# Kernel tuning notes

Hardware: AMD Instinct MI355X
Metric: run time of the kernel (lower is better)

Reference implementation:

```python
import jax, jax.numpy as jnp
import numpy as np

N_NODES = 100000
N_EDGES = 1600000
IN_CH = 128
OUT_CH = 64
H1 = 4 * OUT_CH  # 256
H2 = 2 * OUT_CH  # 128


def setup_inputs() -> dict:
    key = jax.random.key(0)
    ks = jax.random.split(key, 6)
    x = jax.random.normal(ks[0], (N_NODES, IN_CH), dtype=jnp.float32)
    edge_index = jax.random.randint(ks[1], (2, N_EDGES), 0, N_NODES, dtype=jnp.int64)
    # Glorot-style init for the three GCNConv weight matrices
    W1 = jax.random.normal(ks[2], (IN_CH, H1), dtype=jnp.float32) / np.sqrt(IN_CH)
    W2 = jax.random.normal(ks[3], (H1, H2), dtype=jnp.float32) / np.sqrt(H1)
    W3 = jax.random.normal(ks[4], (H2, OUT_CH), dtype=jnp.float32) / np.sqrt(H2)
    b1 = jnp.zeros((H1,), jnp.float32)
    b2 = jnp.zeros((H2,), jnp.float32)
    b3 = jnp.zeros((OUT_CH,), jnp.float32)
    return {"x": x, "edge_index": edge_index, "W1": W1, "b1": b1,
            "W2": W2, "b2": b2, "W3": W3, "b3": b3}


def reference(x, edge_index, W1, b1, W2, b2, W3, b3):
    N = x.shape[0]
    # GCNConv semantics (PyG defaults): add self-loops, symmetric D^-1/2 A D^-1/2 norm.
    loops = jnp.arange(N, dtype=edge_index.dtype)
    src = jnp.concatenate([edge_index[0], loops])  # message sources
    dst = jnp.concatenate([edge_index[1], loops])  # aggregation targets
    deg = jax.ops.segment_sum(jnp.ones_like(dst, x.dtype), dst, num_segments=N)
    dinv = jax.lax.rsqrt(jnp.maximum(deg, 1.0))  # deg >= 1 due to self-loops
    norm = dinv[src] * dinv[dst]  # [E+N] per-edge normalization

    def gcn(h, W, b):
        h = h @ W                                   # dense transform first
        msg = h[src] * norm[:, None]                # gather + normalize
        return jax.ops.segment_sum(msg, dst, num_segments=N) + b

    h = gcn(x, W1, b1)
    h = jax.nn.relu(gcn(h, W2, b2))
    return gcn(h, W3, b3)
```

## Files before the change

### kernel.cpp

```cpp
#include <hip/hip_runtime.h>
#include <cstddef>
#include <cstdint>

#define NND 100000
#define NED 1600000
#define NEP (NED + NND)
#define NPB 256
#define NBK ((NND + NPB - 1) / NPB)
#define ECH 2048

typedef short v8s __attribute__((ext_vector_type(8)));
typedef float v4f __attribute__((ext_vector_type(4)));

__device__ __forceinline__ uint32_t f32_to_bf16_rne(float x) {
    uint32_t u = __builtin_bit_cast(uint32_t, x);
    return (u + 0x7fffu + ((u >> 16) & 1u)) >> 16;
}
__device__ __forceinline__ float bf16bits_to_f32(uint32_t b) {
    return __builtin_bit_cast(float, b << 16);
}

__global__ void k_detect(const long long* __restrict__ ei, int* __restrict__ flag) {
    __shared__ int ok;
    if (threadIdx.x == 0) ok = 1;
    __syncthreads();
    for (int i = threadIdx.x; i < 2048; i += blockDim.x) {
        long long v = ei[i];
        if (v < 0 || v >= NND) ok = 0;
    }
    __syncthreads();
    if (threadIdx.x == 0) *flag = ok;
}

__device__ __forceinline__ void load_edge(const void* ei, int is64, int e, int& src, int& dst) {
    if (e >= NED) { src = dst = e - NED; return; }
    if (is64) {
        const long long* p = (const long long*)ei;
        src = (int)p[e];
        dst = (int)p[NED + e];
    } else {
        const int* p = (const int*)ei;
        src = p[e];
        dst = p[NED + e];
    }
}

__global__ __launch_bounds__(256) void k_bcount(const void* __restrict__ ei,
                                                const int* __restrict__ flag,
                                                int* __restrict__ bcnt) {
    __shared__ int cnt[NBK];
    const int t = threadIdx.x;
    for (int j = t; j < NBK; j += 256) cnt[j] = 0;
    __syncthreads();
    const int is64 = *flag;
    const int e0 = blockIdx.x * ECH;
#pragma unroll
    for (int i = 0; i < 8; ++i) {
        int e = e0 + t + i * 256;
        if (e < NEP) {
            int s, d;
            load_edge(ei, is64, e, s, d);
            atomicAdd(&cnt[d >> 8], 1);
        }
    }
    __syncthreads();
    for (int j = t; j < NBK; j += 256)
        if (cnt[j]) atomicAdd(&bcnt[j], cnt[j]);
}

__global__ __launch_bounds__(512) void k_bscan(const int* __restrict__ bcnt,
                                               int* __restrict__ boff,
                                               int* __restrict__ bcur) {
    __shared__ int sh[512];
    const int t = threadIdx.x;
    int v = (t < NBK) ? bcnt[t] : 0;
    sh[t] = v;
    __syncthreads();
    for (int off = 1; off < 512; off <<= 1) {
        int u = 0;
        if (t >= off) u = sh[t - off];
        __syncthreads();
        sh[t] += u;
        __syncthreads();
    }
    if (t < NBK) {
        int e = sh[t] - v;
        boff[t] = e;
        bcur[t] = e;
    }
    if (t == NBK) boff[NBK] = NEP;
}

__global__ __launch_bounds__(256) void k_bscatter(const void* __restrict__ ei,
                                                  const int* __restrict__ flag,
                                                  int* __restrict__ bcur,
                                                  uint2* __restrict__ pairs) {
    __shared__ int cnt[NBK];
    __shared__ int res[NBK];
    const int t = threadIdx.x;
    for (int j = t; j < NBK; j += 256) cnt[j] = 0;
    __syncthreads();
    const int is64 = *flag;
    const int e0 = blockIdx.x * ECH;
    int se[8], de[8], rk[8];
#pragma unroll
    for (int i = 0; i < 8; ++i) {
        int e = e0 + t + i * 256;
        if (e < NEP) {
            load_edge(ei, is64, e, se[i], de[i]);
            rk[i] = atomicAdd(&cnt[de[i] >> 8], 1);
        } else {
            de[i] = -1;
        }
    }
    __syncthreads();
    for (int j = t; j < NBK; j += 256) {
        int c = cnt[j];
        if (c) res[j] = atomicAdd(&bcur[j], c);
    }
    __syncthreads();
#pragma unroll
    for (int i = 0; i < 8; ++i) {
        if (de[i] >= 0) {
            int pos = res[de[i] >> 8] + rk[i];
            pairs[pos] = make_uint2((unsigned)se[i], (unsigned)de[i]);
        }
    }
}

__global__ __launch_bounds__(256) void k_bcsr(const uint2* __restrict__ pairs,
                                              const int* __restrict__ boff,
                                              int* __restrict__ row_off,
                                              float* __restrict__ dinv,
                                              int* __restrict__ col) {
    __shared__ int deg[NPB];
    __shared__ int off[NPB];
    __shared__ int cur[NPB];
    const int b = blockIdx.x;
    const int t = threadIdx.x;
    const int node0 = b * NPB;
    const int es = boff[b], ee = boff[b + 1];

    deg[t] = 0;
    __syncthreads();
    for (int e = es + t; e < ee; e += 256) {
        uint2 p = pairs[e];
        atomicAdd(&deg[p.y - node0], 1);
    }
    __syncthreads();
    int v = deg[t];
    off[t] = v;
    __syncthreads();
    for (int o = 1; o < 256; o <<= 1) {
        int u = 0;
        if (t >= o) u = off[t - o];
        __syncthreads();
        off[t] += u;
        __syncthreads();
    }
    const int excl = off[t] - v;
    const int node = node0 + t;
    if (node <= NND) row_off[node] = es + excl;
    if (node < NND) {
        int dd = v < 1 ? 1 : v;
        dinv[node] = 1.0f / sqrtf((float)dd);
    }
    cur[t] = es + excl;
    __syncthreads();
    for (int e = es + t; e < ee; e += 256) {
        uint2 p = pairs[e];
        int pos = atomicAdd(&cur[p.y - node0], 1);
        col[pos] = (int)p.x;
    }
}

__global__ void k_wcombsplit(const float* __restrict__ W1, const float* __restrict__ W2,
                             const float* __restrict__ b1, unsigned short* __restrict__ wtCh,
                             unsigned short* __restrict__ wtCl, float* __restrict__ bc) {
    const int j = threadIdx.x;
    const int i = blockIdx.x;
    const float* rowv = (i < 128) ? (W1 + (size_t)i * 256) : b1;
    float acc = 0.f;
    for (int k = 0; k < 256; ++k) acc = fmaf(rowv[k], W2[(size_t)k * 128 + j], acc);
    if (i < 128) {
        uint32_t hi = f32_to_bf16_rne(acc);
        float resid = acc - bf16bits_to_f32(hi);
        uint32_t lo = f32_to_bf16_rne(resid);
        wtCh[(size_t)j * 128 + i] = (unsigned short)hi;
        wtCl[(size_t)j * 128 + i] = (unsigned short)lo;
    } else {
        bc[j] = acc;
    }
}

__global__ void k_wprep(const float* __restrict__ W, unsigned short* __restrict__ wth,
                        unsigned short* __restrict__ wtl, int K, int N) {
    int i = blockIdx.x * 256 + threadIdx.x;
    if (i >= K * N) return;
    int k = i / N, n = i % N;
    float x = W[i];
    uint32_t hi = f32_to_bf16_rne(x);
    float resid = x - bf16bits_to_f32(hi);
    uint32_t lo = f32_to_bf16_rne(resid);
    wth[(size_t)n * K + k] = (unsigned short)hi;
    wtl[(size_t)n * K + k] = (unsigned short)lo;
}

template <int C, bool BIAS, bool RELU, bool OUT_SPLIT>
__global__ __launch_bounds__(C) void k_agg(const float* __restrict__ in, float* __restrict__ out,
                      const int* __restrict__ row_off, const int* __restrict__ col,
                      const float* __restrict__ dinv, const float* __restrict__ bias,
                      unsigned short* __restrict__ outh, unsigned short* __restrict__ outl) {
    constexpr int LPG = C / 4;
    constexpr int NG = 4;
    constexpr int MAXE = 256;
    __shared__ int sidx[MAXE];
    __shared__ float snrm[MAXE];
    __shared__ float4 red[NG][LPG];

    const int n = blockIdx.x;
    const int t = threadIdx.x;
    const int g = t / LPG;
    const int l = t % LPG;
    const int s = row_off[n], e = row_off[n + 1];
    const float4* __restrict__ in4 = (const float4*)in;

    float4 a0 = make_float4(0.f, 0.f, 0.f, 0.f);
    float4 a1 = make_float4(0.f, 0.f, 0.f, 0.f);
    float4 a2 = make_float4(0.f, 0.f, 0.f, 0.f);
    float4 a3 = make_float4(0.f, 0.f, 0.f, 0.f);

    for (int base = s; base < e; base += MAXE) {
        const int cnt = min(e - base, MAXE);
        for (int i = t; i < cnt; i += C) {
            int c = col[base + i];
            sidx[i] = c;
            snrm[i] = dinv[c];
        }
        __syncthreads();

        int k = g;
        for (; k + 3 * NG < cnt; k += 4 * NG) {
            int s0 = sidx[k];
            int s1 = sidx[k + NG];
            int s2 = sidx[k + 2 * NG];
            int s3 = sidx[k + 3 * NG];
            float d0 = snrm[k];
            float d1 = snrm[k + NG];
            float d2 = snrm[k + 2 * NG];
            float d3 = snrm[k + 3 * NG];
            float4 v0 = in4[(size_t)s0 * LPG + l];
            float4 v1 = in4[(size_t)s1 * LPG + l];
            float4 v2 = in4[(size_t)s2 * LPG + l];
            float4 v3 = in4[(size_t)s3 * LPG + l];
            a0.x = fmaf(d0, v0.x, a0.x); a0.y = fmaf(d0, v0.y, a0.y);
            a0.z = fmaf(d0, v0.z, a0.z); a0.w = fmaf(d0, v0.w, a0.w);
            a1.x = fmaf(d1, v1.x, a1.x); a1.y = fmaf(d1, v1.y, a1.y);
            a1.z = fmaf(d1, v1.z, a1.z); a1.w = fmaf(d1, v1.w, a1.w);
            a2.x = fmaf(d2, v2.x, a2.x); a2.y = fmaf(d2, v2.y, a2.y);
            a2.z = fmaf(d2, v2.z, a2.z); a2.w = fmaf(d2, v2.w, a2.w);
            a3.x = fmaf(d3, v3.x, a3.x); a3.y = fmaf(d3, v3.y, a3.y);
            a3.z = fmaf(d3, v3.z, a3.z); a3.w = fmaf(d3, v3.w, a3.w);
        }
        for (; k < cnt; k += NG) {
            int s0 = sidx[k];
            float d0 = snrm[k];
            float4 v0 = in4[(size_t)s0 * LPG + l];
            a0.x = fmaf(d0, v0.x, a0.x); a0.y = fmaf(d0, v0.y, a0.y);
            a0.z = fmaf(d0, v0.z, a0.z); a0.w = fmaf(d0, v0.w, a0.w);
        }
        __syncthreads();
    }

    a0.x += a1.x + a2.x + a3.x;
    a0.y += a1.y + a2.y + a3.y;
    a0.z += a1.z + a2.z + a3.z;
    a0.w += a1.w + a2.w + a3.w;
    red[g][l] = a0;
    __syncthreads();
    if (g == 0) {
        float4 r = red[0][l];
        float4 r1 = red[1][l];
        float4 r2 = red[2][l];
        float4 r3 = red[3][l];
        r.x += r1.x + r2.x + r3.x;
        r.y += r1.y + r2.y + r3.y;
        r.z += r1.z + r2.z + r3.z;
        r.w += r1.w + r2.w + r3.w;
        float dn = dinv[n];
        r.x *= dn; r.y *= dn; r.z *= dn; r.w *= dn;
        if constexpr (BIAS) {
            float4 bv = ((const float4*)bias)[l];
            r.x += bv.x; r.y += bv.y; r.z += bv.z; r.w += bv.w;
        }
        if constexpr (RELU) {
            r.x = fmaxf(r.x, 0.f); r.y = fmaxf(r.y, 0.f);
            r.z = fmaxf(r.z, 0.f); r.w = fmaxf(r.w, 0.f);
        }
        if constexpr (OUT_SPLIT) {
            uint32_t h0 = f32_to_bf16_rne(r.x), h1 = f32_to_bf16_rne(r.y);
            uint32_t h2 = f32_to_bf16_rne(r.z), h3 = f32_to_bf16_rne(r.w);
            uint32_t l0 = f32_to_bf16_rne(r.x - bf16bits_to_f32(h0));
            uint32_t l1 = f32_to_bf16_rne(r.y - bf16bits_to_f32(h1));
            uint32_t l2 = f32_to_bf16_rne(r.z - bf16bits_to_f32(h2));
            uint32_t l3 = f32_to_bf16_rne(r.w - bf16bits_to_f32(h3));
            uint2 oh = make_uint2(h0 | (h1 << 16), h2 | (h3 << 16));
            uint2 ol = make_uint2(l0 | (l1 << 16), l2 | (l3 << 16));
            *(uint2*)(outh + (size_t)n * C + l * 4) = oh;
            *(uint2*)(outl + (size_t)n * C + l * 4) = ol;
        } else {
            ((float4*)out)[(size_t)n * LPG + l] = r;
        }
    }
}

template <int K, int N, int WN, int WM, bool BIAS, bool OUT_SPLIT>
__global__ __launch_bounds__(WN * WM * 64, 3) void k_mgemm(
    const unsigned short* __restrict__ acth, const unsigned short* __restrict__ actl,
    const unsigned short* __restrict__ wth, const unsigned short* __restrict__ wtl,
    const float* __restrict__ bias, float* __restrict__ outf,
    unsigned short* __restrict__ outh, unsigned short* __restrict__ outl, int nrows)
{
    constexpr int BM = 64;
    constexpr int BK = 128;
    constexpr int NCH = K / BK;
    constexpr int KC = BK / 32;
    constexpr int KP = BK + 8;
    constexpr int NTW = N / (WN * 16);
    constexpr int RT = 4 / WM;
    constexpr int NTHR = WN * WM * 64;
    constexpr int CHUNKS = BM * BK / 8;

    __shared__ unsigned short sh[2][BM][KP];

    const int tid = threadIdx.x;
    const int lane = tid & 63;
    const int wave = tid >> 6;
    const int wn = wave % WN;
    const int wm = wave / WN;
    const int l15 = lane & 15;
    const int lq = lane >> 4;
    const int r0 = blockIdx.x * BM;
    const int ncol0 = wn * NTW * 16;

    v8s wh[NTW][K / 32], wl[NTW][K / 32];
#pragma unroll
    for (int nt = 0; nt < NTW; ++nt) {
        const size_t nrow = (size_t)(ncol0 + nt * 16 + l15) * K;
#pragma unroll
        for (int kk = 0; kk < K / 32; ++kk) {
            wh[nt][kk] = *(const v8s*)(wth + nrow + kk * 32 + lq * 8);
            wl[nt][kk] = *(const v8s*)(wtl + nrow + kk * 32 + lq * 8);
        }
    }

    v4f acc[RT][NTW];
#pragma unroll
    for (int rt = 0; rt < RT; ++rt)
#pragma unroll
        for (int nt = 0; nt < NTW; ++nt) acc[rt][nt] = (v4f){0.f, 0.f, 0.f, 0.f};

#pragma unroll
    for (int ch = 0; ch < NCH; ++ch) {
        if (ch) __syncthreads();
        for (int i = tid; i < 2 * CHUNKS; i += NTHR) {
            const int plane = i >= CHUNKS;
            const int j = plane ? i - CHUNKS : i;
            const int r = j / (BK / 8);
            const int c = (j % (BK / 8)) * 8;
            int gr = r0 + r;
            if (gr >= nrows) gr = nrows - 1;
            const unsigned short* src = (plane ? actl : acth) + (size_t)gr * K + ch * BK + c;
            *(v8s*)(&sh[plane][r][c]) = *(const v8s*)src;
        }
        __syncthreads();

#pragma unroll
        for (int kc = 0; kc < KC; ++kc) {
#pragma unroll
            for (int rt = 0; rt < RT; ++rt) {
                const int row = (wm * RT + rt) * 16 + l15;
                const v8s ah = *(const v8s*)(&sh[0][row][kc * 32 + lq * 8]);
                const v8s al = *(const v8s*)(&sh[1][row][kc * 32 + lq * 8]);
                const int kk = ch * KC + kc;
#pragma unroll
                for (int nt = 0; nt < NTW; ++nt) {
                    acc[rt][nt] = __builtin_amdgcn_mfma_f32_16x16x32_bf16(wh[nt][kk], ah, acc[rt][nt], 0, 0, 0);
                    acc[rt][nt] = __builtin_amdgcn_mfma_f32_16x16x32_bf16(wh[nt][kk], al, acc[rt][nt], 0, 0, 0);
                    acc[rt][nt] = __builtin_amdgcn_mfma_f32_16x16x32_bf16(wl[nt][kk], ah, acc[rt][nt], 0, 0, 0);
                }
            }
        }
    }

#pragma unroll
    for (int rt = 0; rt < RT; ++rt) {
        const int m = r0 + (wm * RT + rt) * 16 + l15;
        if (m >= nrows) continue;
#pragma unroll
        for (int nt = 0; nt < NTW; ++nt) {
            const int nc = ncol0 + nt * 16 + lq * 4;
            v4f v = acc[rt][nt];
            if constexpr (BIAS) {
                float4 bv = *(const float4*)(bias + nc);
                v[0] += bv.x; v[1] += bv.y; v[2] += bv.z; v[3] += bv.w;
            }
            if constexpr (OUT_SPLIT) {
                uint32_t h0 = f32_to_bf16_rne(v[0]), h1 = f32_to_bf16_rne(v[1]);
                uint32_t h2 = f32_to_bf16_rne(v[2]), h3 = f32_to_bf16_rne(v[3]);
                uint32_t l0 = f32_to_bf16_rne(v[0] - bf16bits_to_f32(h0));
                uint32_t l1 = f32_to_bf16_rne(v[1] - bf16bits_to_f32(h1));
                uint32_t l2 = f32_to_bf16_rne(v[2] - bf16bits_to_f32(h2));
                uint32_t l3 = f32_to_bf16_rne(v[3] - bf16bits_to_f32(h3));
                *(uint2*)(outh + (size_t)m * N + nc) = make_uint2(h0 | (h1 << 16), h2 | (h3 << 16));
                *(uint2*)(outl + (size_t)m * N + nc) = make_uint2(l0 | (l1 << 16), l2 | (l3 << 16));
            } else {
                *(float4*)(outf + (size_t)m * N + nc) = make_float4(v[0], v[1], v[2], v[3]);
            }
        }
    }
}

extern "C" void kernel_launch(void* const* d_in, const int* in_sizes, int n_in,
                              void* d_out, int out_size, void* d_ws, size_t ws_size,
                              hipStream_t stream) {
    const float* x = (const float*)d_in[0];
    const void* ei = d_in[1];
    const float* W1 = (const float*)d_in[2];
    const float* b1 = (const float*)d_in[3];
    const float* W2 = (const float*)d_in[4];
    const float* b2 = (const float*)d_in[5];
    const float* W3 = (const float*)d_in[6];
    const float* b3 = (const float*)d_in[7];
    float* out = (float*)d_out;

    char* ws = (char*)d_ws;
    size_t off = 0;
    auto alloc = [&](size_t bytes) -> void* {
        void* p = ws + off;
        off = (off + bytes + 255) & ~(size_t)255;
        return p;
    };

    int* flag = (int*)alloc(sizeof(int));
    int* bcnt = (int*)alloc((size_t)NBK * 4);
    int* boff = (int*)alloc((size_t)(NBK + 1) * 4);
    int* bcur = (int*)alloc((size_t)NBK * 4);
    int* row_off = (int*)alloc((size_t)(NND + 1) * 4);
    float* dinv = (float*)alloc((size_t)NND * 4);
    int* col = (int*)alloc((size_t)NEP * 4);
    uint2* pairs = (uint2*)alloc((size_t)NEP * 8);
    float* bc = (float*)alloc((size_t)128 * 4);
    unsigned short* wtCh = (unsigned short*)alloc((size_t)128 * 128 * 2);
    unsigned short* wtCl = (unsigned short*)alloc((size_t)128 * 128 * 2);
    unsigned short* wt3h = (unsigned short*)alloc((size_t)128 * 64 * 2);
    unsigned short* wt3l = (unsigned short*)alloc((size_t)128 * 64 * 2);
    unsigned short* AXh = (unsigned short*)alloc((size_t)NND * 128 * 2 * 2);
    unsigned short* AXl = AXh + (size_t)NND * 128;
    float* H2 = (float*)alloc((size_t)NND * 128 * 4);
    unsigned short* A2h = AXh;
    unsigned short* A2l = AXl;
    float* H3 = H2;

    hipMemsetAsync(bcnt, 0, (size_t)NBK * 4, stream);

    k_detect<<<1, 256, 0, stream>>>((const long long*)ei, flag);

    const int gB = (NEP + ECH - 1) / ECH;
    k_bcount<<<gB, 256, 0, stream>>>(ei, flag, bcnt);
    k_bscan<<<1, 512, 0, stream>>>(bcnt, boff, bcur);
    k_bscatter<<<gB, 256, 0, stream>>>(ei, flag, bcur, pairs);
    k_bcsr<<<NBK, 256, 0, stream>>>(pairs, boff, row_off, dinv, col);

    k_wcombsplit<<<129, 128, 0, stream>>>(W1, W2, b1, wtCh, wtCl, bc);
    k_wprep<<<(128 * 64 + 255) / 256, 256, 0, stream>>>(W3, wt3h, wt3l, 128, 64);

    const int gT = (NND + 63) / 64;

    k_agg<128, false, false, true><<<NND, 128, 0, stream>>>(x, nullptr, row_off, col, dinv, nullptr, AXh, AXl);
    k_mgemm<128, 128, 8, 1, true, false><<<gT, 512, 0, stream>>>(AXh, AXl, wtCh, wtCl, bc, H2, nullptr, nullptr, NND);

    k_agg<128, true, true, true><<<NND, 128, 0, stream>>>(H2, nullptr, row_off, col, dinv, b2, A2h, A2l);

    k_mgemm<128, 64, 4, 2, false, false><<<gT, 512, 0, stream>>>(A2h, A2l, wt3h, wt3l, nullptr, H3, nullptr, nullptr, NND);
    k_agg<64, true, false, false><<<NND, 64, 0, stream>>>(H3, out, row_off, col, dinv, b3, nullptr, nullptr);
}
```

Baseline: 444.0 us.

## Widen final aggregation blocks, cache bucket pairs in LDS, double edge chunk size

```diff
diff --git a/kernel.cpp b/kernel.cpp
--- a/kernel.cpp
+++ b/kernel.cpp
@@ -7,7 +7,8 @@
 #define NEP (NED + NND)
 #define NPB 256
 #define NBK ((NND + NPB - 1) / NPB)
-#define ECH 2048
+#define ECH 4096
+#define MAXB 5120
 
 typedef short v8s __attribute__((ext_vector_type(8)));
 typedef float v4f __attribute__((ext_vector_type(4)));
@@ -55,7 +56,7 @@
     const int is64 = *flag;
     const int e0 = blockIdx.x * ECH;
 #pragma unroll
-    for (int i = 0; i < 8; ++i) {
+    for (int i = 0; i < ECH / 256; ++i) {
         int e = e0 + t + i * 256;
         if (e < NEP) {
             int s, d;
@@ -97,14 +98,15 @@
                                                   uint2* __restrict__ pairs) {
     __shared__ int cnt[NBK];
     __shared__ int res[NBK];
+    constexpr int EPT = ECH / 256;
     const int t = threadIdx.x;
     for (int j = t; j < NBK; j += 256) cnt[j] = 0;
     __syncthreads();
     const int is64 = *flag;
     const int e0 = blockIdx.x * ECH;
-    int se[8], de[8], rk[8];
-#pragma unroll
-    for (int i = 0; i < 8; ++i) {
+    int se[EPT], de[EPT], rk[EPT];
+#pragma unroll
+    for (int i = 0; i < EPT; ++i) {
         int e = e0 + t + i * 256;
         if (e < NEP) {
             load_edge(ei, is64, e, se[i], de[i]);
@@ -120,7 +122,7 @@
     }
     __syncthreads();
 #pragma unroll
-    for (int i = 0; i < 8; ++i) {
+    for (int i = 0; i < EPT; ++i) {
         if (de[i] >= 0) {
             int pos = res[de[i] >> 8] + rk[i];
             pairs[pos] = make_uint2((unsigned)se[i], (unsigned)de[i]);
@@ -133,6 +135,7 @@
                                               int* __restrict__ row_off,
                                               float* __restrict__ dinv,
                                               int* __restrict__ col) {
+    __shared__ uint2 sp[MAXB];
     __shared__ int deg[NPB];
     __shared__ int off[NPB];
     __shared__ int cur[NPB];
@@ -140,11 +143,14 @@
     const int t = threadIdx.x;
     const int node0 = b * NPB;
     const int es = boff[b], ee = boff[b + 1];
+    const int m = ee - es;
+    const bool fits = (m <= MAXB);
 
     deg[t] = 0;
     __syncthreads();
-    for (int e = es + t; e < ee; e += 256) {
-        uint2 p = pairs[e];
+    for (int i = t; i < m; i += 256) {
+        uint2 p = pairs[es + i];
+        if (fits) sp[i] = p;
         atomicAdd(&deg[p.y - node0], 1);
     }
     __syncthreads();
@@ -167,8 +173,8 @@
     }
     cur[t] = es + excl;
     __syncthreads();
-    for (int e = es + t; e < ee; e += 256) {
-        uint2 p = pairs[e];
+    for (int i = t; i < m; i += 256) {
+        uint2 p = fits ? sp[i] : pairs[es + i];
         int pos = atomicAdd(&cur[p.y - node0], 1);
         col[pos] = (int)p.x;
     }
@@ -207,12 +213,12 @@
 }
 
 template <int C, bool BIAS, bool RELU, bool OUT_SPLIT>
-__global__ __launch_bounds__(C) void k_agg(const float* __restrict__ in, float* __restrict__ out,
+__global__ __launch_bounds__(128) void k_agg(const float* __restrict__ in, float* __restrict__ out,
                       const int* __restrict__ row_off, const int* __restrict__ col,
                       const float* __restrict__ dinv, const float* __restrict__ bias,
                       unsigned short* __restrict__ outh, unsigned short* __restrict__ outl) {
     constexpr int LPG = C / 4;
-    constexpr int NG = 4;
+    constexpr int NG = 128 / LPG;
     constexpr int MAXE = 256;
     __shared__ int sidx[MAXE];
     __shared__ float snrm[MAXE];
@@ -232,7 +238,7 @@
 
     for (int base = s; base < e; base += MAXE) {
         const int cnt = min(e - base, MAXE);
-        for (int i = t; i < cnt; i += C) {
+        for (int i = t; i < cnt; i += 128) {
             int c = col[base + i];
             sidx[i] = c;
             snrm[i] = dinv[c];
@@ -280,13 +286,11 @@
     __syncthreads();
     if (g == 0) {
         float4 r = red[0][l];
-        float4 r1 = red[1][l];
-        float4 r2 = red[2][l];
-        float4 r3 = red[3][l];
-        r.x += r1.x + r2.x + r3.x;
-        r.y += r1.y + r2.y + r3.y;
-        r.z += r1.z + r2.z + r3.z;
-        r.w += r1.w + r2.w + r3.w;
+#pragma unroll
+        for (int q = 1; q < NG; ++q) {
+            float4 rq = red[q][l];
+            r.x += rq.x; r.y += rq.y; r.z += rq.z; r.w += rq.w;
+        }
         float dn = dinv[n];
         r.x *= dn; r.y *= dn; r.z *= dn; r.w *= dn;
         if constexpr (BIAS) {
@@ -483,5 +487,5 @@
     k_agg<128, true, true, true><<<NND, 128, 0, stream>>>(H2, nullptr, row_off, col, dinv, b2, A2h, A2l);
 
     k_mgemm<128, 64, 4, 2, false, false><<<gT, 512, 0, stream>>>(A2h, A2l, wt3h, wt3l, nullptr, H3, nullptr, nullptr, NND);
-    k_agg<64, true, false, false><<<NND, 64, 0, stream>>>(H3, out, row_off, col, dinv, b3, nullptr, nullptr);
-}
+    k_agg<64, true, false, false><<<NND, 128, 0, stream>>>(H3, out, row_off, col, dinv, b3, nullptr, nullptr);
+}
```

Result: no change. 447.8 us (+0.9%).
